# Optimization experiments

Hardware: AMD Instinct MI355X
Metric: run time of the kernel (lower is better)

The kernel has to match this reference:

```python
import jax, jax.numpy as jnp
import numpy as np

B, CIN, H, W = 64, 1, 64, 64
L = 6            # layer_number -> 2^L = 64 blocks per axis
T = 4            # chebyshev_number
C4 = 4 * T * T   # per-block channel width = 64
WK = H // 2 ** (L - 1)  # first-layer kernel/stride = 2
LEFT = H // 2 ** L      # leftover_x = leftover_y = 1


def setup_inputs() -> dict:
    key = jax.random.key(0)
    ks = jax.random.split(key, 16)
    d = {}
    d["x_real"] = jax.random.normal(ks[0], (B, CIN, H, W), jnp.float32)
    d["x_imag"] = jax.random.normal(ks[1], (B, CIN, H, W), jnp.float32)
    # layer 0: per-input-channel conv, 4 -> 4*C4 channels, kernel=stride=WK
    d["w0"] = jax.random.normal(ks[2], (CIN, 4 * C4, 4, WK, WK), jnp.float32) / float(np.sqrt(4 * WK * WK))
    d["b0"] = jnp.zeros((CIN, 4 * C4), jnp.float32)
    # recursion layers lyr=1..L-1: one conv per (channel, block), C4 -> 4*C4, kernel 2x2 stride 2
    for lyr in range(1, L):
        G = 2 ** lyr
        d["w%d" % lyr] = jax.random.normal(ks[2 + lyr], (CIN, G, G, 4 * C4, C4, 2, 2), jnp.float32) / float(np.sqrt(4 * C4))
        d["b%d" % lyr] = jnp.zeros((CIN, G, G, 4 * C4), jnp.float32)
    # final layer: 1x1 conv per block, C4 -> 4*LEFT*LEFT
    GL = 2 ** L
    d["wf"] = jax.random.normal(ks[10], (CIN, GL, GL, 4 * LEFT * LEFT, C4), jnp.float32) / float(np.sqrt(C4))
    d["bf"] = jnp.zeros((CIN, GL, GL, 4 * LEFT * LEFT), jnp.float32)
    return d


def _forward(x_real, x_imag, w0, b0, wrec, brec, wf, bf):
    # split(): [relu(re), relu(im), relu(-re), relu(-im)] per input channel
    xs = jax.nn.relu(jnp.stack([x_real, x_imag, -x_real, -x_imag], axis=2))  # (B,CIN,4,H,W)
    # layer 0: kernel=stride=WK conv as blocked einsum -> (B,CIN,4*C4,P,P), P = 2^(L-1)
    P = H // WK
    xb = xs.reshape(B, CIN, 4, P, WK, P, WK)
    y = jnp.einsum('bcipkql,coikl->bcopq', xb, w0) + b0[None, :, :, None, None]
    y = jax.nn.relu(y)
    # output channels = 2x2 block grid x C4; layout (B,CIN,gy,gx,C4,S,S)
    G, S = 2, P
    y = y.reshape(B, CIN, G, G, C4, S, S)
    for lyr in range(1, L):
        w, b = wrec[lyr - 1], brec[lyr - 1]
        S2 = S // 2
        # 2x2/stride-2 conv per block as batched einsum
        yb = y.reshape(B, CIN, G, G, C4, S2, 2, S2, 2)
        z = jnp.einsum('bcghipkql,cghoikl->bcghopq', yb, w) + b[None, :, :, :, :, None, None]
        z = jax.nn.relu(z)
        # out channels split into (y_loc,x_loc,C4); child block = (2*gy+y_loc, 2*gx+x_loc)
        z = z.reshape(B, CIN, G, G, 2, 2, C4, S2, S2)
        z = z.transpose(0, 1, 2, 4, 3, 5, 6, 7, 8).reshape(B, CIN, 2 * G, 2 * G, C4, S2, S2)
        y, G, S = z, 2 * G, S2
    # final layer: spatial S == 1, 1x1 conv per block
    yv = y[..., 0, 0]                                     # (B,CIN,GL,GL,C4)
    f = jnp.einsum('bcghi,cghoi->bcgho', yv, wf) + bf[None]
    f = jax.nn.relu(f)
    # out channel o = 4*(ky*LEFT+kx)+comp; pixel = (gy*LEFT+ky, gx*LEFT+kx)
    f = f.reshape(B, CIN, G, G, LEFT, LEFT, 4)
    f = f.transpose(0, 1, 2, 4, 3, 5, 6).reshape(B, CIN, H, W, 4)
    # joint(): real = comp0 - comp2, then scale by 1/(H*W)
    return (f[..., 0] - f[..., 2]) / (H * W)


def reference(x_real, x_imag, w0, b0, w1, b1, w2, b2, w3, b3, w4, b4, w5, b5, wf, bf):
    return _forward(x_real, x_imag, w0, b0, (w1, w2, w3, w4, w5), (b1, b2, b3, b4, b5), wf, bf)
```

## Files before the change

kernel.cpp:

```cpp
#include <hip/hip_runtime.h>
#include <cstddef>


typedef unsigned int  u32;
typedef unsigned short u16;
typedef __attribute__((ext_vector_type(8))) short bf16x8;
typedef __attribute__((ext_vector_type(4))) float f32x4;

#define PLANE 16777216

__device__ inline u16 bf16_rn(float x) {
    u32 u = __builtin_bit_cast(u32, x);
    u32 r = (u + 0x7FFFu + ((u >> 16) & 1u)) >> 16;
    return (u16)r;
}
__device__ inline float bf16_to_f(u16 h) {
    u32 u = ((u32)h) << 16;
    return __builtin_bit_cast(float, u);
}
__device__ inline u32 pack_split(float v) {
    const u16 h = bf16_rn(v);
    const u16 l = bf16_rn(v - bf16_to_f(h));
    return (u32)h | ((u32)l << 16);
}
__device__ inline void bar_lds() {
    asm volatile("s_waitcnt lgkmcnt(0)\n\ts_barrier" ::: "memory");
}

__global__ __launch_bounds__(256)
void wconv_all_kernel(const float* __restrict__ s1, const float* __restrict__ s2,
                      const float* __restrict__ s3,
                      u16* __restrict__ d1, u16* __restrict__ d2, u16* __restrict__ d3) {
    const int i = blockIdx.x * 256 + threadIdx.x;
    const float* s; u16 *dh, *dl; int off;
    if (i < 32768)        { s = s1; dh = d1; dl = d1 + 262144;  off = i; }
    else if (i < 163840)  { s = s2; dh = d2; dl = d2 + 1048576; off = i - 32768; }
    else                  { s = s3; dh = d3; dl = d3 + 4194304; off = i - 163840; }
    const float4 a = *(const float4*)(s + 8 * off);
    const float4 b = *(const float4*)(s + 8 * off + 4);
    union { bf16x8 v; u16 u[8]; } H, L;
    const float f[8] = {a.x, a.y, a.z, a.w, b.x, b.y, b.z, b.w};
#pragma unroll
    for (int e = 0; e < 8; ++e) {
        const u16 h = bf16_rn(f[e]);
        H.u[e] = h;
        L.u[e] = bf16_rn(f[e] - bf16_to_f(h));
    }
    *(bf16x8*)(dh + 8 * off) = H.v;
    *(bf16x8*)(dl + 8 * off) = L.v;
}

__global__ __launch_bounds__(256)
void layer0_kernel(const float* __restrict__ xr, const float* __restrict__ xi,
                   const float* __restrict__ w0, const float* __restrict__ b0,
                   u32* __restrict__ A1) {
    __shared__ float w0s[128][16];
    __shared__ float b0s[128];
    const int og  = blockIdx.y;
    const int tid = threadIdx.x;
    {
        const int row = tid >> 1, half = tid & 1;
        const float4 wa = *(const float4*)(w0 + (og * 128 + row) * 16 + half * 8);
        const float4 wb = *(const float4*)(w0 + (og * 128 + row) * 16 + half * 8 + 4);
        *(float4*)&w0s[row][half * 8]     = wa;
        *(float4*)&w0s[row][half * 8 + 4] = wb;
        if (tid < 128) b0s[tid] = b0[og * 128 + tid];
    }
    __syncthreads();

    const int n = blockIdx.x * 256 + tid;
    const int b = n >> 10, p = (n >> 5) & 31, q = n & 31;
    float xs[16];
#pragma unroll
    for (int k = 0; k < 2; ++k) {
        const float2 vr = *(const float2*)(xr + b * 4096 + (2 * p + k) * 64 + 2 * q);
        const float2 vi = *(const float2*)(xi + b * 4096 + (2 * p + k) * 64 + 2 * q);
        xs[0  + k * 2 + 0] = fmaxf(vr.x, 0.f);  xs[0  + k * 2 + 1] = fmaxf(vr.y, 0.f);
        xs[4  + k * 2 + 0] = fmaxf(vi.x, 0.f);  xs[4  + k * 2 + 1] = fmaxf(vi.y, 0.f);
        xs[8  + k * 2 + 0] = fmaxf(-vr.x, 0.f); xs[8  + k * 2 + 1] = fmaxf(-vr.y, 0.f);
        xs[12 + k * 2 + 0] = fmaxf(-vi.x, 0.f); xs[12 + k * 2 + 1] = fmaxf(-vi.y, 0.f);
    }
    const int kp = p & 1, lp = q & 1, pp = p >> 1, qp = q >> 1;
    const size_t pixoff = (size_t)(b * 256 + pp * 16 + qp);
#pragma unroll
    for (int j = 0; j < 128; ++j) {
        float acc = b0s[j];
#pragma unroll
        for (int e = 0; e < 16; ++e) acc = fmaf(xs[e], w0s[j][e], acc);
        acc = fmaxf(acc, 0.f);
        const int o = og * 128 + j;
        const int gy = o >> 7, gx = (o >> 6) & 1, c = o & 63;
        const size_t flat = (size_t)((((gy * 2 + gx) * 64 + c) * 2 + kp) * 2 + lp) * (64 * 256)
                          + pixoff;
        A1[flat] = pack_split(acc);
    }
}

template<int NT>
__global__ __launch_bounds__(256, 2)
void rec_mfma_kernel(const u32* __restrict__ Yg,
                     const u16* __restrict__ Whi_g, const u16* __restrict__ Wlo_g,
                     const float* __restrict__ bias, u32* __restrict__ Aout,
                     const int lgG, const int lgS2) {
    constexpr int NF  = NT / 16;
    constexpr int LD  = 40;
    constexpr int NCP = NT / 2;
    constexpr int RPT = 32 / (256 / NCP);

    __shared__ u16 Yhi_s[NT * LD];
    __shared__ u16 Ylo_s[NT * LD];

    const int G  = 1 << lgG;
    const int S2 = 1 << lgS2;
    const int Nb = 64 << (2 * lgS2);

    int bid, nt;
    const int nBid = G * G, NTILES = gridDim.x;
    if (nBid >= 8) {
        const int h = blockIdx.z * NTILES + blockIdx.x;
        const int xcd = h & 7, j = h >> 3, per = nBid >> 3;
        bid = xcd * per + j / NTILES;
        nt  = j % NTILES;
    } else { bid = blockIdx.z; nt = blockIdx.x; }

    const size_t wbase = (size_t)bid * 65536;
    const u32* Yblk = Yg + (size_t)bid * 256 * (size_t)Nb + (size_t)nt * NT;

    const int tid = threadIdx.x, wave = tid >> 6, lane = tid & 63;
    const int l16 = lane & 15, lk = lane >> 4;
    const int cp = tid % NCP, rg = tid / NCP;
    const int col0 = cp * 2, trow = rg * RPT;

    f32x4 acc[4][NF];
#pragma unroll
    for (int m = 0; m < 4; ++m)
#pragma unroll
        for (int n = 0; n < NF; ++n)
            acc[m][n] = (f32x4){0.f, 0.f, 0.f, 0.f};

    uint2  yreg[2][RPT];
    bf16x8 wh[4], wl[4];
    u32 yhw[2][RPT / 2], ylw[2][RPT / 2];

    auto loadY = [&](int ybuf, int k0) {
#pragma unroll
        for (int r = 0; r < RPT; ++r)
            yreg[ybuf][r] = *(const uint2*)(Yblk + (size_t)(k0 + trow + r) * Nb + col0);
    };
    auto loadWpre = [&](int k0) {
#pragma unroll
        for (int m = 0; m < 4; ++m) {
            const size_t off = wbase + (size_t)(wave * 64 + m * 16 + l16) * 256 + k0 + lk * 8;
            wh[m] = *(const bf16x8*)(Whi_g + off);
            wl[m] = *(const bf16x8*)(Wlo_g + off);
        }
    };
    auto prepY = [&](int ybuf) {
#pragma unroll
        for (int c = 0; c < 2; ++c)
#pragma unroll
            for (int j2 = 0; j2 < RPT / 2; ++j2) {
                const u32 a = c ? yreg[ybuf][2 * j2].y     : yreg[ybuf][2 * j2].x;
                const u32 b = c ? yreg[ybuf][2 * j2 + 1].y : yreg[ybuf][2 * j2 + 1].x;
                yhw[c][j2] = (a & 0xFFFFu) | (b << 16);
                ylw[c][j2] = (a >> 16)     | (b & 0xFFFF0000u);
            }
    };
    auto stageY = [&]() {
#pragma unroll
        for (int c = 0; c < 2; ++c) {
            if constexpr (RPT == 8) {
                *(uint4*)&Yhi_s[(col0 + c) * LD + trow] = make_uint4(yhw[c][0], yhw[c][1], yhw[c][2], yhw[c][3]);
                *(uint4*)&Ylo_s[(col0 + c) * LD + trow] = make_uint4(ylw[c][0], ylw[c][1], ylw[c][2], ylw[c][3]);
            } else {
                *(uint2*)&Yhi_s[(col0 + c) * LD + trow] = make_uint2(yhw[c][0], yhw[c][1]);
                *(uint2*)&Ylo_s[(col0 + c) * LD + trow] = make_uint2(ylw[c][0], ylw[c][1]);
            }
        }
    };

    loadY(0, 0); loadY(1, 32);

#pragma unroll
    for (int it = 0; it < 8; ++it) {
        const int k0 = it * 32;
        const int cur = it & 1;
        loadWpre(k0);
        prepY(cur);
        bar_lds();
        stageY();
        bar_lds();
        if (it + 2 < 8) loadY(cur, k0 + 64);
        __builtin_amdgcn_s_setprio(1);
#pragma unroll
        for (int n = 0; n < NF; ++n) {
            const int ccol = n * 16 + l16;
            const bf16x8 bhi = *(const bf16x8*)&Yhi_s[ccol * LD + 8 * lk];
            const bf16x8 blo = *(const bf16x8*)&Ylo_s[ccol * LD + 8 * lk];
#pragma unroll
            for (int m = 0; m < 4; ++m)
                acc[m][n] = __builtin_amdgcn_mfma_f32_16x16x32_bf16(wh[m], bhi, acc[m][n], 0, 0, 0);
#pragma unroll
            for (int m = 0; m < 4; ++m)
                acc[m][n] = __builtin_amdgcn_mfma_f32_16x16x32_bf16(wh[m], blo, acc[m][n], 0, 0, 0);
#pragma unroll
            for (int m = 0; m < 4; ++m)
                acc[m][n] = __builtin_amdgcn_mfma_f32_16x16x32_bf16(wl[m], bhi, acc[m][n], 0, 0, 0);
        }
        __builtin_amdgcn_s_setprio(0);
    }

    const int gy = bid >> lgG, gx = bid & (G - 1);
    const int NS2 = S2 >> 1;
#pragma unroll
    for (int m = 0; m < 4; ++m) {
#pragma unroll
        for (int r = 0; r < 4; ++r) {
            const int oc = wave * 64 + m * 16 + lk * 4 + r;
            const float bi = bias[(size_t)bid * 256 + oc];
            const int yl = oc >> 7, xl = (oc >> 6) & 1, cch = oc & 63;
            const int cy = 2 * gy + yl, cx = 2 * gx + xl;
            const size_t base = (size_t)((cy * (2 * G) + cx) * 64 + cch);
#pragma unroll
            for (int n = 0; n < NF; ++n) {
                const float v = fmaxf(acc[m][n][r] + bi, 0.f);
                const int ng = nt * NT + n * 16 + l16;
                const int b   = ng >> (2 * lgS2);
                const int rem = ng & ((1 << (2 * lgS2)) - 1);
                const int p = rem >> lgS2, q = rem & (S2 - 1);
                const size_t flat = ((base * 2 + (p & 1)) * 2 + (q & 1)) * (size_t)(64 * NS2 * NS2)
                                  + (size_t)(b * NS2 * NS2 + (p >> 1) * NS2 + (q >> 1));
                Aout[flat] = pack_split(v);
            }
        }
    }
}

__global__ __launch_bounds__(256, 2)
void rec45_final_kernel(const u32* __restrict__ Yg, const float* __restrict__ W4,
                        const float* __restrict__ b4, const float* __restrict__ W5,
                        const float* __restrict__ b5, const float* __restrict__ wf,
                        const float* __restrict__ bff, float* __restrict__ out) {
    constexpr int LDW = 72;
    __shared__ u16 Whi_w[64 * LDW];
    __shared__ u16 Wlo_w[64 * LDW];

    const int h = blockIdx.x;
    const int parent = ((h >> 5) << 3) | (h & 7);
    const int child  = (h >> 3) & 3;
    const int pgy = parent >> 4, pgx = parent & 15;
    const int cy = 2 * pgy + (child >> 1), cx = 2 * pgx + (child & 1);
    const int bid5 = cy * 32 + cx;
    const int ocbase = child * 64;

    const u32* Yblk  = Yg + (size_t)parent * 65536;
    const float* W4s = W4 + (size_t)parent * 65536 + (size_t)ocbase * 256;
    const float* W5b = W5 + (size_t)bid5 * 65536;

    const int tid = threadIdx.x, wave = tid >> 6, lane = tid & 63;
    const int l16 = lane & 15, lk = lane >> 4;

    f32x4 acc1[4][4];
#pragma unroll
    for (int m = 0; m < 4; ++m)
#pragma unroll
        for (int n = 0; n < 4; ++n)
            acc1[m][n] = (f32x4){0.f, 0.f, 0.f, 0.f};

    u32    yf[2][4][8];
    float4 wv[2][8];
    bf16x8 wh[4], wl[4];

    auto loadY = [&](int buf, int k0) {
#pragma unroll
        for (int n = 0; n < 4; ++n)
#pragma unroll
            for (int j = 0; j < 8; ++j)
                yf[buf][n][j] = Yblk[(size_t)(k0 + 8 * lk + j) * 256 + wave * 64 + n * 16 + l16];
    };
    auto loadW4 = [&](int buf, int k0) {
#pragma unroll
        for (int m = 0; m < 4; ++m) {
            const float* p = W4s + (size_t)(m * 16 + l16) * 256 + k0 + lk * 8;
            wv[buf][2 * m]     = *(const float4*)p;
            wv[buf][2 * m + 1] = *(const float4*)(p + 4);
        }
    };
    auto loadW5 = [&](int buf, int t) {
#pragma unroll
        for (int m = 0; m < 4; ++m) {
            const float* p = W5b + (size_t)(wave * 64 + m * 16 + l16) * 256 + t * 32 + lk * 8;
            wv[buf][2 * m]     = *(const float4*)p;
            wv[buf][2 * m + 1] = *(const float4*)(p + 4);
        }
    };
    auto convW = [&](int buf) {
#pragma unroll
        for (int m = 0; m < 4; ++m) {
            const float f[8] = { wv[buf][2 * m].x,     wv[buf][2 * m].y,
                                 wv[buf][2 * m].z,     wv[buf][2 * m].w,
                                 wv[buf][2 * m + 1].x, wv[buf][2 * m + 1].y,
                                 wv[buf][2 * m + 1].z, wv[buf][2 * m + 1].w };
            union { bf16x8 v; u16 u[8]; } H, L;
#pragma unroll
            for (int e = 0; e < 8; ++e) {
                const u16 hh = bf16_rn(f[e]);
                H.u[e] = hh;
                L.u[e] = bf16_rn(f[e] - bf16_to_f(hh));
            }
            wh[m] = H.v;
            wl[m] = L.v;
        }
    };

    loadY(0, 0); loadW4(0, 0); loadY(1, 32); loadW4(1, 32);
#pragma unroll
    for (int it = 0; it < 8; ++it) {
        const int cur = it & 1;
        convW(cur);
        __builtin_amdgcn_s_setprio(1);
#pragma unroll
        for (int n = 0; n < 4; ++n) {
            union { bf16x8 v; u16 u[8]; } BH, BL;
#pragma unroll
            for (int j = 0; j < 8; ++j) {
                const u32 y = yf[cur][n][j];
                BH.u[j] = (u16)y;
                BL.u[j] = (u16)(y >> 16);
            }
#pragma unroll
            for (int m = 0; m < 4; ++m)
                acc1[m][n] = __builtin_amdgcn_mfma_f32_16x16x32_bf16(wh[m], BH.v, acc1[m][n], 0, 0, 0);
#pragma unroll
            for (int m = 0; m < 4; ++m)
                acc1[m][n] = __builtin_amdgcn_mfma_f32_16x16x32_bf16(wh[m], BL.v, acc1[m][n], 0, 0, 0);
#pragma unroll
            for (int m = 0; m < 4; ++m)
                acc1[m][n] = __builtin_amdgcn_mfma_f32_16x16x32_bf16(wl[m], BH.v, acc1[m][n], 0, 0, 0);
        }
        __builtin_amdgcn_s_setprio(0);
        if (it + 2 < 8) { loadY(cur, 32 * it + 64); loadW4(cur, 32 * it + 64); }
    }

    f32x4 acc2[4][4];
#pragma unroll
    for (int m = 0; m < 4; ++m)
#pragma unroll
        for (int n = 0; n < 4; ++n)
            acc2[m][n] = (f32x4){0.f, 0.f, 0.f, 0.f};

    float b4v[4][4];
#pragma unroll
    for (int kw = 0; kw < 4; ++kw)
#pragma unroll
        for (int r = 0; r < 4; ++r)
            b4v[kw][r] = b4[(size_t)parent * 256 + ocbase + kw * 16 + lk * 4 + r];

    loadW5(0, 0); loadW5(1, 1);

#pragma unroll
    for (int kw = 0; kw < 4; ++kw) {
#pragma unroll
        for (int n = 0; n < 4; ++n) {
            const int colg = wave * 64 + n * 16 + l16;
            const int b_ = colg >> 2, par = colg & 3;
#pragma unroll
            for (int r = 0; r < 4; ++r) {
                const float v = fmaxf(acc1[kw][n][r] + b4v[kw][r], 0.f);
                const int k_ = lk * 16 + r * 4 + par;
                const u16 hh = bf16_rn(v);
                Whi_w[b_ * LDW + k_] = hh;
                Wlo_w[b_ * LDW + k_] = bf16_rn(v - bf16_to_f(hh));
            }
        }
        bar_lds();
#pragma unroll
        for (int kc = 0; kc < 2; ++kc) {
            const int t = kw * 2 + kc;
            const int cur = t & 1;
            convW(cur);
            __builtin_amdgcn_s_setprio(1);
#pragma unroll
            for (int n = 0; n < 4; ++n) {
                const int b_ = n * 16 + l16;
                const bf16x8 bhi = *(const bf16x8*)&Whi_w[b_ * LDW + kc * 32 + 8 * lk];
                const bf16x8 blo = *(const bf16x8*)&Wlo_w[b_ * LDW + kc * 32 + 8 * lk];
#pragma unroll
                for (int m = 0; m < 4; ++m)
                    acc2[m][n] = __builtin_amdgcn_mfma_f32_16x16x32_bf16(wh[m], bhi, acc2[m][n], 0, 0, 0);
#pragma unroll
                for (int m = 0; m < 4; ++m)
                    acc2[m][n] = __builtin_amdgcn_mfma_f32_16x16x32_bf16(wh[m], blo, acc2[m][n], 0, 0, 0);
#pragma unroll
                for (int m = 0; m < 4; ++m)
                    acc2[m][n] = __builtin_amdgcn_mfma_f32_16x16x32_bf16(wl[m], bhi, acc2[m][n], 0, 0, 0);
            }
            __builtin_amdgcn_s_setprio(0);
            if (t + 2 < 8) loadW5(cur, t + 2);
        }
        bar_lds();
    }

    const int fy = 2 * cy + (wave >> 1), fx = 2 * cx + (wave & 1);
    const int blk = fy * 64 + fx;
    float wf0v[4][4], wf2v[4][4], biv[4][4];
#pragma unroll
    for (int m = 0; m < 4; ++m)
#pragma unroll
        for (int r = 0; r < 4; ++r) {
            const int cch = m * 16 + lk * 4 + r;
            wf0v[m][r] = wf[(size_t)blk * 256 + cch];
            wf2v[m][r] = wf[(size_t)blk * 256 + 128 + cch];
            biv[m][r]  = b5[(size_t)bid5 * 256 + wave * 64 + cch];
        }
    const float bf0 = bff[blk * 4 + 0], bf2 = bff[blk * 4 + 2];
#pragma unroll
    for (int n = 0; n < 4; ++n) {
        float a0 = 0.f, a2 = 0.f;
#pragma unroll
        for (int m = 0; m < 4; ++m)
#pragma unroll
            for (int r = 0; r < 4; ++r) {
                const float y = fmaxf(acc2[m][n][r] + biv[m][r], 0.f);
                a0 = fmaf(y, wf0v[m][r], a0);
                a2 = fmaf(y, wf2v[m][r], a2);
            }
        a0 += __shfl_xor(a0, 16); a0 += __shfl_xor(a0, 32);
        a2 += __shfl_xor(a2, 16); a2 += __shfl_xor(a2, 32);
        if (lk == n) {
            const float o0 = fmaxf(a0 + bf0, 0.f);
            const float o2 = fmaxf(a2 + bf2, 0.f);
            out[(size_t)(n * 16 + l16) * 4096 + blk] = (o0 - o2) * (1.0f / 4096.0f);
        }
    }
}

extern "C" void kernel_launch(void* const* d_in, const int* in_sizes, int n_in,
                              void* d_out, int out_size, void* d_ws, size_t ws_size,
                              hipStream_t stream) {
    (void)in_sizes; (void)n_in; (void)out_size; (void)ws_size;

    const float* xr = (const float*)d_in[0];
    const float* xi = (const float*)d_in[1];
    const float* w0 = (const float*)d_in[2];
    const float* b0 = (const float*)d_in[3];
    const float* wrec[5] = { (const float*)d_in[4],  (const float*)d_in[6],
                             (const float*)d_in[8],  (const float*)d_in[10],
                             (const float*)d_in[12] };
    const float* brec[5] = { (const float*)d_in[5],  (const float*)d_in[7],
                             (const float*)d_in[9],  (const float*)d_in[11],
                             (const float*)d_in[13] };
    const float* wf = (const float*)d_in[14];
    const float* bf = (const float*)d_in[15];
    float* out = (float*)d_out;

    u32* bufA = (u32*)d_ws;
    u32* bufB = bufA + (size_t)PLANE;
    u16* wc1  = (u16*)(bufB + (size_t)PLANE);
    u16* wc2  = wc1 + (size_t)2 * 262144;
    u16* wc3  = wc2 + (size_t)2 * 1048576;

    wconv_all_kernel<<<2688, 256, 0, stream>>>(wrec[0], wrec[1], wrec[2], wc1, wc2, wc3);

    layer0_kernel<<<dim3(256, 2), 256, 0, stream>>>(xr, xi, w0, b0, bufA);

    rec_mfma_kernel<128><<<dim3(128, 1, 4), 256, 0, stream>>>(
        bufA, wc1, wc1 + 262144, brec[0], bufB, 1, 4);
    rec_mfma_kernel<128><<<dim3(32, 1, 16), 256, 0, stream>>>(
        bufB, wc2, wc2 + 1048576, brec[1], bufA, 2, 3);
    rec_mfma_kernel<128><<<dim3(8, 1, 64), 256, 0, stream>>>(
        bufA, wc3, wc3 + 4194304, brec[2], bufB, 3, 2);
    rec45_final_kernel<<<1024, 256, 0, stream>>>(
        bufB, wrec[3], brec[3], wrec[4], brec[4], wf, bf, out);
}
```

Baseline: 270.6 us.

## Double-buffer LDS staging and prefetch weights earlier in recursion kernels

In the recursion MFMA kernel, the Y tile is now staged into two LDS buffers, so the next tile is written while the current one is consumed, and the global Y prefetch runs one step further ahead. This drops one barrier per iteration. In the fused layer-4/5 kernel, the intermediate weight tile is also double-buffered in LDS, and the W4/W5 global loads are issued before the MFMA block instead of after it, so they overlap with compute. The cost is twice the LDS footprint and more live registers, which could lower occupancy under the launch bounds of 2.

```diff
diff --git a/kernel.cpp b/kernel.cpp
--- a/kernel.cpp
+++ b/kernel.cpp
@@ -107,8 +107,8 @@
     constexpr int NCP = NT / 2;
     constexpr int RPT = 32 / (256 / NCP);
 
-    __shared__ u16 Yhi_s[NT * LD];
-    __shared__ u16 Ylo_s[NT * LD];
+    __shared__ u16 Yhi_s[2][NT * LD];
+    __shared__ u16 Ylo_s[2][NT * LD];
 
     const int G  = 1 << lgG;
     const int S2 = 1 << lgS2;
@@ -140,7 +140,6 @@
 
     uint2  yreg[2][RPT];
     bf16x8 wh[4], wl[4];
-    u32 yhw[2][RPT / 2], ylw[2][RPT / 2];
 
     auto loadY = [&](int ybuf, int k0) {
 #pragma unroll
@@ -155,7 +154,8 @@
             wl[m] = *(const bf16x8*)(Wlo_g + off);
         }
     };
-    auto prepY = [&](int ybuf) {
+    auto prepstage = [&](int ybuf, int sbuf) {
+        u32 yhw[2][RPT / 2], ylw[2][RPT / 2];
 #pragma unroll
         for (int c = 0; c < 2; ++c)
 #pragma unroll
@@ -165,38 +165,36 @@
                 yhw[c][j2] = (a & 0xFFFFu) | (b << 16);
                 ylw[c][j2] = (a >> 16)     | (b & 0xFFFF0000u);
             }
-    };
-    auto stageY = [&]() {
 #pragma unroll
         for (int c = 0; c < 2; ++c) {
             if constexpr (RPT == 8) {
-                *(uint4*)&Yhi_s[(col0 + c) * LD + trow] = make_uint4(yhw[c][0], yhw[c][1], yhw[c][2], yhw[c][3]);
-                *(uint4*)&Ylo_s[(col0 + c) * LD + trow] = make_uint4(ylw[c][0], ylw[c][1], ylw[c][2], ylw[c][3]);
+                *(uint4*)&Yhi_s[sbuf][(col0 + c) * LD + trow] = make_uint4(yhw[c][0], yhw[c][1], yhw[c][2], yhw[c][3]);
+                *(uint4*)&Ylo_s[sbuf][(col0 + c) * LD + trow] = make_uint4(ylw[c][0], ylw[c][1], ylw[c][2], ylw[c][3]);
             } else {
-                *(uint2*)&Yhi_s[(col0 + c) * LD + trow] = make_uint2(yhw[c][0], yhw[c][1]);
-                *(uint2*)&Ylo_s[(col0 + c) * LD + trow] = make_uint2(ylw[c][0], ylw[c][1]);
+                *(uint2*)&Yhi_s[sbuf][(col0 + c) * LD + trow] = make_uint2(yhw[c][0], yhw[c][1]);
+                *(uint2*)&Ylo_s[sbuf][(col0 + c) * LD + trow] = make_uint2(ylw[c][0], ylw[c][1]);
             }
         }
     };
 
     loadY(0, 0); loadY(1, 32);
+    prepstage(0, 0);
+    loadY(0, 64);
 
 #pragma unroll
     for (int it = 0; it < 8; ++it) {
         const int k0 = it * 32;
-        const int cur = it & 1;
+        const int sb = it & 1;
         loadWpre(k0);
-        prepY(cur);
         bar_lds();
-        stageY();
-        bar_lds();
-        if (it + 2 < 8) loadY(cur, k0 + 64);
+        if (it + 1 < 8) prepstage((it + 1) & 1, sb ^ 1);
+        if (it + 3 < 8) loadY((it + 1) & 1, 32 * (it + 3));
         __builtin_amdgcn_s_setprio(1);
 #pragma unroll
         for (int n = 0; n < NF; ++n) {
             const int ccol = n * 16 + l16;
-            const bf16x8 bhi = *(const bf16x8*)&Yhi_s[ccol * LD + 8 * lk];
-            const bf16x8 blo = *(const bf16x8*)&Ylo_s[ccol * LD + 8 * lk];
+            const bf16x8 bhi = *(const bf16x8*)&Yhi_s[sb][ccol * LD + 8 * lk];
+            const bf16x8 blo = *(const bf16x8*)&Ylo_s[sb][ccol * LD + 8 * lk];
 #pragma unroll
             for (int m = 0; m < 4; ++m)
                 acc[m][n] = __builtin_amdgcn_mfma_f32_16x16x32_bf16(wh[m], bhi, acc[m][n], 0, 0, 0);
@@ -242,8 +240,8 @@
                         const float* __restrict__ b5, const float* __restrict__ wf,
                         const float* __restrict__ bff, float* __restrict__ out) {
     constexpr int LDW = 72;
-    __shared__ u16 Whi_w[64 * LDW];
-    __shared__ u16 Wlo_w[64 * LDW];
+    __shared__ u16 Whi_w[2][64 * LDW];
+    __shared__ u16 Wlo_w[2][64 * LDW];
 
     const int h = blockIdx.x;
     const int parent = ((h >> 5) << 3) | (h & 7);
@@ -318,6 +316,8 @@
     for (int it = 0; it < 8; ++it) {
         const int cur = it & 1;
         convW(cur);
+        if (it + 2 < 8) loadW4(cur, 32 * it + 64);
+        else            loadW5(cur, it - 6);
         __builtin_amdgcn_s_setprio(1);
 #pragma unroll
         for (int n = 0; n < 4; ++n) {
@@ -339,7 +339,7 @@
                 acc1[m][n] = __builtin_amdgcn_mfma_f32_16x16x32_bf16(wl[m], BH.v, acc1[m][n], 0, 0, 0);
         }
         __builtin_amdgcn_s_setprio(0);
-        if (it + 2 < 8) { loadY(cur, 32 * it + 64); loadW4(cur, 32 * it + 64); }
+        if (it + 2 < 8) loadY(cur, 32 * it + 64);
     }
 
     f32x4 acc2[4][4];
@@ -356,10 +356,7 @@
         for (int r = 0; r < 4; ++r)
             b4v[kw][r] = b4[(size_t)parent * 256 + ocbase + kw * 16 + lk * 4 + r];
 
-    loadW5(0, 0); loadW5(1, 1);
-
-#pragma unroll
-    for (int kw = 0; kw < 4; ++kw) {
+    auto writeWin = [&](int kw, int wb) {
 #pragma unroll
         for (int n = 0; n < 4; ++n) {
             const int colg = wave * 64 + n * 16 + l16;
@@ -369,22 +366,31 @@
                 const float v = fmaxf(acc1[kw][n][r] + b4v[kw][r], 0.f);
                 const int k_ = lk * 16 + r * 4 + par;
                 const u16 hh = bf16_rn(v);
-                Whi_w[b_ * LDW + k_] = hh;
-                Wlo_w[b_ * LDW + k_] = bf16_rn(v - bf16_to_f(hh));
-            }
-        }
+                Whi_w[wb][b_ * LDW + k_] = hh;
+                Wlo_w[wb][b_ * LDW + k_] = bf16_rn(v - bf16_to_f(hh));
+            }
+        }
+    };
+
+    writeWin(0, 0);
+
+#pragma unroll
+    for (int kw = 0; kw < 4; ++kw) {
+        const int wb = kw & 1;
         bar_lds();
+        if (kw + 1 < 4) writeWin(kw + 1, wb ^ 1);
 #pragma unroll
         for (int kc = 0; kc < 2; ++kc) {
             const int t = kw * 2 + kc;
             const int cur = t & 1;
             convW(cur);
+            if (t + 2 < 8) loadW5(cur, t + 2);
             __builtin_amdgcn_s_setprio(1);
 #pragma unroll
             for (int n = 0; n < 4; ++n) {
                 const int b_ = n * 16 + l16;
-                const bf16x8 bhi = *(const bf16x8*)&Whi_w[b_ * LDW + kc * 32 + 8 * lk];
-                const bf16x8 blo = *(const bf16x8*)&Wlo_w[b_ * LDW + kc * 32 + 8 * lk];
+                const bf16x8 bhi = *(const bf16x8*)&Whi_w[wb][b_ * LDW + kc * 32 + 8 * lk];
+                const bf16x8 blo = *(const bf16x8*)&Wlo_w[wb][b_ * LDW + kc * 32 + 8 * lk];
 #pragma unroll
                 for (int m = 0; m < 4; ++m)
                     acc2[m][n] = __builtin_amdgcn_mfma_f32_16x16x32_bf16(wh[m], bhi, acc2[m][n], 0, 0, 0);
@@ -396,9 +402,7 @@
                     acc2[m][n] = __builtin_amdgcn_mfma_f32_16x16x32_bf16(wl[m], bhi, acc2[m][n], 0, 0, 0);
             }
             __builtin_amdgcn_s_setprio(0);
-            if (t + 2 < 8) loadW5(cur, t + 2);
-        }
-        bar_lds();
+        }
     }
 
     const int fy = 2 * cy + (wave >> 1), fx = 2 * cx + (wave & 1);
```

Result: slower. 287.0 us (+6.1%).
